# Performance work log

Measured on AMD Instinct MI355X. Metric: run time of the kernel, lower is better.

## Reference

```python
import jax, jax.numpy as jnp
import numpy as np

C = 256
RED = 8
D = C // RED  # qk dim = 32
EPS = 1e-5   # nn.LayerNorm default


def setup_inputs() -> dict:
    key = jax.random.key(0)
    ks = jax.random.split(key, 10)
    B, H, W = 4, 64, 64
    s = 0.02
    return {
        "x": jax.random.normal(ks[0], (B, C, H, W), dtype=jnp.float32),
        "wq": jax.random.normal(ks[1], (D, C), dtype=jnp.float32) * s,
        "bq": jax.random.normal(ks[2], (D,), dtype=jnp.float32) * s,
        "wk": jax.random.normal(ks[3], (D, C), dtype=jnp.float32) * s,
        "bk": jax.random.normal(ks[4], (D,), dtype=jnp.float32) * s,
        "wv": jax.random.normal(ks[5], (C, C), dtype=jnp.float32) * s,
        "bv": jax.random.normal(ks[6], (C,), dtype=jnp.float32) * s,
        "gamma": jax.random.normal(ks[7], (1,), dtype=jnp.float32) * 0.1,
        "ln_w": jnp.ones((C,), dtype=jnp.float32),
        "ln_b": jnp.zeros((C,), dtype=jnp.float32),
    }


def reference(x, wq, bq, wk, bk, wv, bv, gamma, ln_w, ln_b):
    B, Cc, H, W = x.shape
    N = H * W
    xf = x.reshape(B, Cc, N)  # [B,C,N]
    # 1x1 convs == per-pixel linear over channels
    q = jnp.einsum('dc,bcn->bnd', wq, xf) + bq              # [B,N,D]
    k = jnp.einsum('dc,bcn->bdn', wk, xf) + bk[:, None]     # [B,D,N]
    v = jnp.einsum('ec,bcn->ben', wv, xf) + bv[:, None]     # [B,C,N]
    scale = 1.0 / (D ** 0.5)
    scores = jnp.einsum('bnd,bdm->bnm', q, k) * scale       # [B,N,N]
    # original subtracts row max then softmax; jax.nn.softmax is equivalent & stable
    attn = jax.nn.softmax(scores, axis=-1)                  # [B,N,N]
    out = jnp.einsum('bcm,bnm->bcn', v, attn)               # [B,C,N]
    res = gamma[0] * out + xf                               # gamma residual
    # LayerNorm over channel dim (module permutes to channels-last)
    r = res.transpose(0, 2, 1)                              # [B,N,C]
    mu = jnp.mean(r, axis=-1, keepdims=True)
    var = jnp.mean(jnp.square(r - mu), axis=-1, keepdims=True)
    y = (r - mu) * jax.lax.rsqrt(var + EPS) * ln_w + ln_b
    return y.transpose(0, 2, 1).reshape(B, Cc, H, W)
```

## Files before the change

### kernel.cpp

```cpp
#include <hip/hip_runtime.h>
#include <hip/hip_bf16.h>

#define NPIX 4096
#define NCH  256

typedef __attribute__((ext_vector_type(8))) short short8;
typedef __attribute__((ext_vector_type(4))) short s16x4;
typedef __attribute__((ext_vector_type(16))) float f32x16;
typedef __attribute__((ext_vector_type(8))) int i32x8;

union Frag64 { long l[4]; i32x8 v; };

#define SC1 0x7F7F7F7F

__device__ inline unsigned int pkfp8x4(float a, float b, float c, float d) {
    int w = __builtin_amdgcn_cvt_pk_fp8_f32(a, b, 0, false);
    w = __builtin_amdgcn_cvt_pk_fp8_f32(c, d, w, true);
    return (unsigned int)w;
}

__device__ inline unsigned char fp8b(float a) {
    return (unsigned char)(__builtin_amdgcn_cvt_pk_fp8_f32(a, a, 0, false) & 0xff);
}

__device__ inline float bperm(int srclane, float v) {
    return __int_as_float(__builtin_amdgcn_ds_bpermute(
        srclane << 2, __float_as_int(v)));
}

__device__ inline unsigned short bfbits(float f) {
    __hip_bfloat16 h = __float2bfloat16(f);
    return *reinterpret_cast<unsigned short*>(&h);
}

#if __has_builtin(__builtin_amdgcn_exp2f)
__device__ inline float exp2_raw(float x) { return __builtin_amdgcn_exp2f(x); }
#else
__device__ inline float exp2_raw(float x) { return __builtin_exp2f(x); }
#endif

__device__ inline void barrier_nodrain() {
    __builtin_amdgcn_sched_barrier(0);
    asm volatile("s_waitcnt lgkmcnt(0)" ::: "memory");
    __builtin_amdgcn_s_barrier();
    __builtin_amdgcn_sched_barrier(0);
}

__global__ void __launch_bounds__(256) prep_kernel(
    const float* __restrict__ x,
    const float* __restrict__ wq, const float* __restrict__ bq,
    const float* __restrict__ wk, const float* __restrict__ bk,
    const float* __restrict__ wv, const float* __restrict__ bv,
    __hip_bfloat16* __restrict__ Wc, float* __restrict__ bc,
    __hip_bfloat16* __restrict__ XTg)
{
    const int bid = blockIdx.x;
    const int t   = threadIdx.x;
    if (bid >= 1024) {
        const int j = bid - 1024;
        const float kQ = 0.17677669529663687f * 1.4426950408889634f;
        const float* src;
        float sc = 1.0f;
        if (j < 32)       { src = wq + j * 256; }
        else if (j < 64)  { src = wk + (j - 32) * 256; sc = kQ; }
        else              { src = wv + (j - 64) * 256; }
        Wc[j * 256 + t] = __float2bfloat16(src[t] * sc);
        if (t == 0) {
            float bb = (j < 32) ? bq[j] : (j < 64) ? bk[j - 32] * kQ : bv[j - 64];
            bc[j] = bb;
        }
        return;
    }
    __shared__ float xs[64][65];
    const int b  = bid >> 8;
    const int c0 = ((bid >> 6) & 3) * 64;
    const int n0 = (bid & 63) * 64;
    const float* xb = x + ((size_t)b * NCH + c0) * NPIX + n0;
    #pragma unroll
    for (int i = 0; i < 4; ++i) {
        int c  = i * 16 + (t >> 4);
        int n4 = (t & 15) * 4;
        float4 v = *(const float4*)(xb + (size_t)c * NPIX + n4);
        xs[c][n4 + 0] = v.x;
        xs[c][n4 + 1] = v.y;
        xs[c][n4 + 2] = v.z;
        xs[c][n4 + 3] = v.w;
    }
    __syncthreads();
    #pragma unroll
    for (int i = 0; i < 4; ++i) {
        int nn  = i * 16 + (t >> 4);
        int cL4 = (t & 15) * 4;
        s16x4 w;
        w.x = (short)bfbits(xs[cL4 + 0][nn]);
        w.y = (short)bfbits(xs[cL4 + 1][nn]);
        w.z = (short)bfbits(xs[cL4 + 2][nn]);
        w.w = (short)bfbits(xs[cL4 + 3][nn]);
        *(s16x4*)(XTg + ((size_t)b * NPIX + n0 + nn) * NCH + c0 + cL4) = w;
    }
}

__global__ void __launch_bounds__(256) proj_kernel(
    const __hip_bfloat16* __restrict__ Wc, const float* __restrict__ bc,
    const __hip_bfloat16* __restrict__ XTg,
    unsigned char* __restrict__ Q8, unsigned char* __restrict__ K8,
    unsigned char* __restrict__ V8)
{
    const int b    = blockIdx.z;
    const int t    = threadIdx.x;
    const int lane = t & 63;
    const int wid  = t >> 6;
    const int lo   = lane & 31;
    const int hi   = lane >> 5;
    const int n0   = blockIdx.x * 128 + wid * 32;
    const int jb   = blockIdx.y * 2;

    short8 xf[16];
    const __hip_bfloat16* xr = XTg + ((size_t)b * NPIX + n0 + lo) * NCH;
    #pragma unroll
    for (int ks = 0; ks < 16; ++ks)
        xf[ks] = *(const short8*)(xr + ks * 16 + hi * 8);

    #pragma unroll
    for (int jo = 0; jo < 2; ++jo) {
        const int jt = jb + jo;
        f32x16 acc;
        #pragma unroll
        for (int r = 0; r < 16; ++r) acc[r] = 0.f;
        const __hip_bfloat16* wr = Wc + (size_t)(jt * 32 + lo) * NCH;
        #pragma unroll
        for (int ks = 0; ks < 16; ++ks) {
            short8 wf = *(const short8*)(wr + ks * 16 + hi * 8);
            acc = __builtin_amdgcn_mfma_f32_32x32x16_bf16(wf, xf[ks], acc, 0, 0, 0);
        }
        if (jt < 2) {
            unsigned char* dst = (jt == 0 ? Q8 : K8)
                               + ((size_t)b * NPIX + n0 + lo) * 32;
            #pragma unroll
            for (int g = 0; g < 4; ++g) {
                int jr = 8 * g + 4 * hi;
                unsigned int w = pkfp8x4(acc[4 * g + 0] + bc[jt * 32 + jr + 0],
                                         acc[4 * g + 1] + bc[jt * 32 + jr + 1],
                                         acc[4 * g + 2] + bc[jt * 32 + jr + 2],
                                         acc[4 * g + 3] + bc[jt * 32 + jr + 3]);
                *(unsigned int*)(dst + jr) = w;
            }
        } else {
            unsigned char* vb = V8 + (size_t)b * NPIX * NCH
                              + (size_t)((n0 + lo) >> 4) * 4096 + (lo & 15);
            #pragma unroll
            for (int r = 0; r < 16; ++r) {
                int jr = (r & 3) + 8 * (r >> 2) + 4 * hi;
                int c  = jt * 32 + jr - 64;
                vb[(size_t)c * 16] = fp8b(acc[r] + bc[jt * 32 + jr]);
            }
        }
    }
}

__global__ void __launch_bounds__(512, 4) attn_kernel(
    const unsigned char* __restrict__ Q8, const unsigned char* __restrict__ K8,
    const unsigned char* __restrict__ V8, const __hip_bfloat16* __restrict__ XTg,
    const float* __restrict__ gamma_p, const float* __restrict__ lnw,
    const float* __restrict__ lnb, float* __restrict__ out)
{
    __shared__ char smem[39936];

    const int t    = threadIdx.x;
    const int lane = t & 63;
    const int wid  = __builtin_amdgcn_readfirstlane(t >> 6);
    const int lo   = lane & 31;
    const int hi   = lane >> 5;

    const int lid = blockIdx.y * 128 + blockIdx.x;
    const int xcd = lid & 7;
    const int b   = xcd >> 1;
    const int q0  = ((xcd & 1) * 64 + (lid >> 3)) * 32;

    const unsigned char* Qb = Q8 + ((size_t)b * NPIX + q0) * 32;
    Frag64 qv;
    qv.l[0] = *(const long*)(Qb + lo * 32 + hi * 8);
    qv.l[1] = *(const long*)(Qb + lo * 32 + 16 + hi * 8);
    qv.l[2] = 0; qv.l[3] = 0;

    const unsigned char* Ku = K8 + (size_t)b * NPIX * 32 + wid * 1024;
    const int koff = lo * 32 + hi * 8;
    const unsigned char* Vu = V8 + (size_t)b * NPIX * NCH + wid * 512;
    const int vloff = lo * 16 + hi * 8;

    unsigned int rva[16];
    #pragma unroll
    for (int s = 0; s < 4; ++s)
        #pragma unroll
        for (int p = 0; p < 4; ++p)
            rva[4 * s + p] = (unsigned)(lo * 256
                           + (((8 * s + 2 * p + hi) ^ (lo & 15)) << 3));
    unsigned int wva[4];
    #pragma unroll
    for (int g = 0; g < 4; ++g)
        wva[g] = (unsigned)(lo * 256 + 4 * hi
               + (((4 * wid + g) ^ (lo & 15)) << 3));

    f32x16 acc;
    #pragma unroll
    for (int r = 0; r < 16; ++r) acc[r] = 0.f;
    float s_run = 0.f;

    Frag64 ka;
    ka.l[0] = *(const long*)(Ku + koff);
    ka.l[1] = *(const long*)(Ku + koff + 16);
    ka.l[2] = 0; ka.l[3] = 0;
    long kB0 = 0, kB1 = 0;

    Frag64 vva[4];
    #pragma unroll
    for (int s = 0; s < 4; ++s)
        #pragma unroll
        for (int p = 0; p < 4; ++p)
            vva[s].l[p] = *(const long*)(Vu + (4 * s + p) * 4096 + vloff);

    {
        f32x16 sct;
        #pragma unroll
        for (int r = 0; r < 16; ++r) sct[r] = 0.f;
        sct = __builtin_amdgcn_mfma_scale_f32_32x32x64_f8f6f4(
            ka.v, qv.v, sct, 0, 0, 0, SC1, 0, SC1);
        kB0 = *(const long*)(Ku + 8192 + koff);
        kB1 = *(const long*)(Ku + 8192 + koff + 16);
        float psum = 0.f;
        #pragma unroll
        for (int g = 0; g < 4; ++g) {
            float e0 = exp2_raw(sct[4 * g + 0]);
            float e1 = exp2_raw(sct[4 * g + 1]);
            float e2 = exp2_raw(sct[4 * g + 2]);
            float e3 = exp2_raw(sct[4 * g + 3]);
            psum += (e0 + e1) + (e2 + e3);
            *(unsigned int*)(smem + wva[g]) = pkfp8x4(e0, e1, e2, e3);
        }
        s_run += psum;
    }
    barrier_nodrain();

    for (int it = 1; it < 16; ++it) {
        #pragma unroll
        for (int g = 0; g < 4; ++g) wva[g] ^= 8192u;

        ka.l[0] = kB0; ka.l[1] = kB1;
        f32x16 sct;
        #pragma unroll
        for (int r = 0; r < 16; ++r) sct[r] = 0.f;
        sct = __builtin_amdgcn_mfma_scale_f32_32x32x64_f8f6f4(
            ka.v, qv.v, sct, 0, 0, 0, SC1, 0, SC1);

        __builtin_amdgcn_s_setprio(1);
        #pragma unroll
        for (int s = 0; s < 4; ++s) {
            Frag64 pa;
            #pragma unroll
            for (int p = 0; p < 4; ++p)
                pa.l[p] = *(const long*)(smem + rva[4 * s + p]);
            acc = __builtin_amdgcn_mfma_scale_f32_32x32x64_f8f6f4(
                pa.v, vva[s].v, acc, 0, 0, 0, SC1, 0, SC1);
        }
        __builtin_amdgcn_s_setprio(0);

        if (it < 15) {
            const unsigned char* kn = Ku + (size_t)(it + 1) * 8192;
            kB0 = *(const long*)(kn + koff);
            kB1 = *(const long*)(kn + koff + 16);
        }

        const unsigned char* vit = Vu + (size_t)it * 65536;
        #pragma unroll
        for (int s = 0; s < 4; ++s)
            #pragma unroll
            for (int p = 0; p < 4; ++p)
                vva[s].l[p] = *(const long*)(vit + (4 * s + p) * 4096 + vloff);

        float psum = 0.f;
        #pragma unroll
        for (int g = 0; g < 4; ++g) {
            float e0 = exp2_raw(sct[4 * g + 0]);
            float e1 = exp2_raw(sct[4 * g + 1]);
            float e2 = exp2_raw(sct[4 * g + 2]);
            float e3 = exp2_raw(sct[4 * g + 3]);
            psum += (e0 + e1) + (e2 + e3);
            *(unsigned int*)(smem + wva[g]) = pkfp8x4(e0, e1, e2, e3);
        }
        s_run += psum;

        barrier_nodrain();

        #pragma unroll
        for (int i = 0; i < 16; ++i) rva[i] ^= 8192u;
    }

    {
        __builtin_amdgcn_s_setprio(1);
        #pragma unroll
        for (int s = 0; s < 4; ++s) {
            Frag64 pa;
            #pragma unroll
            for (int p = 0; p < 4; ++p)
                pa.l[p] = *(const long*)(smem + rva[4 * s + p]);
            acc = __builtin_amdgcn_mfma_scale_f32_32x32x64_f8f6f4(
                pa.v, vva[s].v, acc, 0, 0, 0, SC1, 0, SC1);
        }
        __builtin_amdgcn_s_setprio(0);
    }

    s_run += __shfl_xor(s_run, 32);

    float* red_sp = (float*)(smem + 36864);
    float* red2p  = (float*)(smem + 37888);
    float (*ybuf)[36] = (float(*)[36])smem;

    if (hi == 0) red_sp[wid * 32 + lo] = s_run;
    __syncthreads();
    float stot = 0.f;
    #pragma unroll
    for (int w = 0; w < 8; ++w) stot += red_sp[w * 32 + lo];
    const float invs = 1.0f / stot;
    const float gamma = gamma_p[0];
    const int cL = 32 * wid + lo;
    const __hip_bfloat16* XTb = XTg + ((size_t)b * NPIX + q0) * NCH + cL;
    float rv[16];
    #pragma unroll
    for (int r = 0; r < 16; ++r) {
        int qr = (r & 3) + 8 * (r >> 2) + 4 * hi;
        float ir = bperm(qr, invs);
        float xv = __bfloat162float(XTb[(size_t)qr * NCH]);
        rv[r] = gamma * (acc[r] * ir) + xv;
        float s1 = rv[r];
        float s2 = rv[r] * rv[r];
        #pragma unroll
        for (int off = 1; off < 32; off <<= 1) {
            s1 += __shfl_xor(s1, off);
            s2 += __shfl_xor(s2, off);
        }
        if (lo == 0) {
            red2p[qr * 16 + wid * 2]     = s1;
            red2p[qr * 16 + wid * 2 + 1] = s2;
        }
    }
    __syncthreads();
    float sA = 0.f, sB = 0.f;
    #pragma unroll
    for (int w = 0; w < 8; ++w) {
        sA += red2p[lo * 16 + w * 2];
        sB += red2p[lo * 16 + w * 2 + 1];
    }
    const float mean = sA * (1.f / 256.f);
    const float var  = sB * (1.f / 256.f) - mean * mean;
    const float rstd = rsqrtf(var + 1e-5f);
    const float lwv = lnw[cL];
    const float lbv = lnb[cL];
    #pragma unroll
    for (int r = 0; r < 16; ++r) {
        int qr = (r & 3) + 8 * (r >> 2) + 4 * hi;
        float m  = bperm(qr, mean);
        float rr = bperm(qr, rstd);
        ybuf[cL][qr] = (rv[r] - m) * rr * lwv + lbv;
    }
    __syncthreads();
    const int c_r = t >> 1;
    const int qh  = (t & 1) * 16;
    float* dst = out + ((size_t)b * NCH + c_r) * NPIX + q0 + qh;
    #pragma unroll
    for (int j = 0; j < 4; ++j) {
        float4 v;
        v.x = ybuf[c_r][qh + j * 4 + 0];
        v.y = ybuf[c_r][qh + j * 4 + 1];
        v.z = ybuf[c_r][qh + j * 4 + 2];
        v.w = ybuf[c_r][qh + j * 4 + 3];
        *(float4*)(dst + j * 4) = v;
    }
}

extern "C" void kernel_launch(void* const* d_in, const int* in_sizes, int n_in,
                              void* d_out, int out_size, void* d_ws, size_t ws_size,
                              hipStream_t stream) {
    const float* x     = (const float*)d_in[0];
    const float* wq    = (const float*)d_in[1];
    const float* bq    = (const float*)d_in[2];
    const float* wk    = (const float*)d_in[3];
    const float* bk    = (const float*)d_in[4];
    const float* wv    = (const float*)d_in[5];
    const float* bv    = (const float*)d_in[6];
    const float* gamma = (const float*)d_in[7];
    const float* ln_w  = (const float*)d_in[8];
    const float* ln_b  = (const float*)d_in[9];
    float* out = (float*)d_out;

    const int B = 4;
    unsigned char* ws = (unsigned char*)d_ws;
    unsigned char*  Q8 = ws;
    unsigned char*  K8 = ws + (512u << 10);
    unsigned char*  V8 = ws + (1u << 20);
    __hip_bfloat16* XT = (__hip_bfloat16*)(ws + (5u << 20));
    __hip_bfloat16* Wc = (__hip_bfloat16*)(ws + (13u << 20));
    float*          bc = (float*)(ws + (13u << 20) + 163840);

    prep_kernel<<<dim3(1344), 256, 0, stream>>>(x, wq, bq, wk, bk, wv, bv,
                                                Wc, bc, XT);
    proj_kernel<<<dim3(32, 5, B), 256, 0, stream>>>(Wc, bc, XT, Q8, K8, V8);
    attn_kernel<<<dim3(128, B), 512, 0, stream>>>(Q8, K8, V8, XT, gamma,
                                                  ln_w, ln_b, out);
}
```

Measured before the change: 85.91 us.

## Process two key sub-blocks per barrier stage to halve synchronization count

The attention main loop now handles 512 keys per stage instead of 256, running two QK MFMA/exp sub-steps and two PV sub-steps between barriers, so it takes 8 iterations instead of 16. The K prefetch covers two fragments and the LDS probability buffer doubles its row stride and double-buffer offset. The aim is to halve the block barriers and the per-stage overhead, and to interleave more independent work for latency hiding. In exchange it uses more LDS and registers, which may lower occupancy and pushes the scratch reduction region close to the larger buffer.

Measured after the change: 119.4 us. 38.9% more time.

```diff
diff --git a/kernel.cpp b/kernel.cpp
--- a/kernel.cpp
+++ b/kernel.cpp
@@ -183,50 +183,56 @@
     qv.l[1] = *(const long*)(Qb + lo * 32 + 16 + hi * 8);
     qv.l[2] = 0; qv.l[3] = 0;
 
-    const unsigned char* Ku = K8 + (size_t)b * NPIX * 32 + wid * 1024;
+    const unsigned char* Ku = K8 + (size_t)b * NPIX * 32 + wid * 2048;
     const int koff = lo * 32 + hi * 8;
     const unsigned char* Vu = V8 + (size_t)b * NPIX * NCH + wid * 512;
     const int vloff = lo * 16 + hi * 8;
 
+    const int swz = lo & 15;
     unsigned int rva[16];
     #pragma unroll
     for (int s = 0; s < 4; ++s)
         #pragma unroll
         for (int p = 0; p < 4; ++p)
-            rva[4 * s + p] = (unsigned)(lo * 256
-                           + (((8 * s + 2 * p + hi) ^ (lo & 15)) << 3));
-    unsigned int wva[4];
-    #pragma unroll
-    for (int g = 0; g < 4; ++g)
-        wva[g] = (unsigned)(lo * 256 + 4 * hi
-               + (((4 * wid + g) ^ (lo & 15)) << 3));
+            rva[4 * s + p] = (unsigned)(lo * 512
+                           + (((8 * s + 2 * p + hi) ^ swz) << 3));
+    unsigned int wva[8];
+    #pragma unroll
+    for (int g = 0; g < 8; ++g)
+        wva[g] = (unsigned)(lo * 512 + 4 * hi
+               + (((8 * wid + g) ^ swz) << 3));
 
     f32x16 acc;
     #pragma unroll
     for (int r = 0; r < 16; ++r) acc[r] = 0.f;
     float s_run = 0.f;
 
-    Frag64 ka;
-    ka.l[0] = *(const long*)(Ku + koff);
-    ka.l[1] = *(const long*)(Ku + koff + 16);
-    ka.l[2] = 0; ka.l[3] = 0;
-    long kB0 = 0, kB1 = 0;
+    Frag64 ka0, ka1;
+    ka0.l[0] = *(const long*)(Ku + koff);
+    ka0.l[1] = *(const long*)(Ku + koff + 16);
+    ka0.l[2] = 0; ka0.l[3] = 0;
+    ka1.l[0] = *(const long*)(Ku + 1024 + koff);
+    ka1.l[1] = *(const long*)(Ku + 1024 + koff + 16);
+    ka1.l[2] = 0; ka1.l[3] = 0;
+    long kB0 = 0, kB1 = 0, kB2 = 0, kB3 = 0;
 
     Frag64 vva[4];
     #pragma unroll
     for (int s = 0; s < 4; ++s)
         #pragma unroll
         for (int p = 0; p < 4; ++p)
-            vva[s].l[p] = *(const long*)(Vu + (4 * s + p) * 4096 + vloff);
+            vva[s].l[p] = *(const long*)(Vu + s * 16384 + p * 4096 + vloff);
 
     {
         f32x16 sct;
         #pragma unroll
         for (int r = 0; r < 16; ++r) sct[r] = 0.f;
         sct = __builtin_amdgcn_mfma_scale_f32_32x32x64_f8f6f4(
-            ka.v, qv.v, sct, 0, 0, 0, SC1, 0, SC1);
-        kB0 = *(const long*)(Ku + 8192 + koff);
-        kB1 = *(const long*)(Ku + 8192 + koff + 16);
+            ka0.v, qv.v, sct, 0, 0, 0, SC1, 0, SC1);
+        kB0 = *(const long*)(Ku + 16384 + koff);
+        kB1 = *(const long*)(Ku + 16384 + koff + 16);
+        kB2 = *(const long*)(Ku + 16384 + 1024 + koff);
+        kB3 = *(const long*)(Ku + 16384 + 1024 + koff + 16);
         float psum = 0.f;
         #pragma unroll
         for (int g = 0; g < 4; ++g) {
@@ -237,20 +243,35 @@
             psum += (e0 + e1) + (e2 + e3);
             *(unsigned int*)(smem + wva[g]) = pkfp8x4(e0, e1, e2, e3);
         }
-        s_run += psum;
-    }
-    barrier_nodrain();
-
-    for (int it = 1; it < 16; ++it) {
-        #pragma unroll
-        for (int g = 0; g < 4; ++g) wva[g] ^= 8192u;
-
-        ka.l[0] = kB0; ka.l[1] = kB1;
-        f32x16 sct;
         #pragma unroll
         for (int r = 0; r < 16; ++r) sct[r] = 0.f;
         sct = __builtin_amdgcn_mfma_scale_f32_32x32x64_f8f6f4(
-            ka.v, qv.v, sct, 0, 0, 0, SC1, 0, SC1);
+            ka1.v, qv.v, sct, 0, 0, 0, SC1, 0, SC1);
+        #pragma unroll
+        for (int g = 0; g < 4; ++g) {
+            float e0 = exp2_raw(sct[4 * g + 0]);
+            float e1 = exp2_raw(sct[4 * g + 1]);
+            float e2 = exp2_raw(sct[4 * g + 2]);
+            float e3 = exp2_raw(sct[4 * g + 3]);
+            psum += (e0 + e1) + (e2 + e3);
+            *(unsigned int*)(smem + wva[4 + g]) = pkfp8x4(e0, e1, e2, e3);
+        }
+        s_run += psum;
+    }
+    barrier_nodrain();
+
+    for (int it = 1; it < 8; ++it) {
+        #pragma unroll
+        for (int g = 0; g < 8; ++g) wva[g] ^= 16384u;
+
+        ka0.l[0] = kB0; ka0.l[1] = kB1;
+        ka1.l[0] = kB2; ka1.l[1] = kB3;
+
+        f32x16 sct;
+        #pragma unroll
+        for (int r = 0; r < 16; ++r) sct[r] = 0.f;
+        sct = __builtin_amdgcn_mfma_scale_f32_32x32x64_f8f6f4(
+            ka0.v, qv.v, sct, 0, 0, 0, SC1, 0, SC1);
 
         __builtin_amdgcn_s_setprio(1);
         #pragma unroll
@@ -264,18 +285,14 @@
         }
         __builtin_amdgcn_s_setprio(0);
 
-        if (it < 15) {
-            const unsigned char* kn = Ku + (size_t)(it + 1) * 8192;
-            kB0 = *(const long*)(kn + koff);
-            kB1 = *(const long*)(kn + koff + 16);
-        }
-
-        const unsigned char* vit = Vu + (size_t)it * 65536;
-        #pragma unroll
-        for (int s = 0; s < 4; ++s)
-            #pragma unroll
-            for (int p = 0; p < 4; ++p)
-                vva[s].l[p] = *(const long*)(vit + (4 * s + p) * 4096 + vloff);
+        {
+            const unsigned char* vb1 = Vu + (size_t)(it - 1) * 131072 + 65536;
+            #pragma unroll
+            for (int s = 0; s < 4; ++s)
+                #pragma unroll
+                for (int p = 0; p < 4; ++p)
+                    vva[s].l[p] = *(const long*)(vb1 + s * 16384 + p * 4096 + vloff);
+        }
 
         float psum = 0.f;
         #pragma unroll
@@ -287,12 +304,56 @@
             psum += (e0 + e1) + (e2 + e3);
             *(unsigned int*)(smem + wva[g]) = pkfp8x4(e0, e1, e2, e3);
         }
+
+        #pragma unroll
+        for (int r = 0; r < 16; ++r) sct[r] = 0.f;
+        sct = __builtin_amdgcn_mfma_scale_f32_32x32x64_f8f6f4(
+            ka1.v, qv.v, sct, 0, 0, 0, SC1, 0, SC1);
+
+        __builtin_amdgcn_s_setprio(1);
+        #pragma unroll
+        for (int s = 0; s < 4; ++s) {
+            Frag64 pa;
+            #pragma unroll
+            for (int p = 0; p < 4; ++p)
+                pa.l[p] = *(const long*)(smem + rva[4 * s + p] + 256);
+            acc = __builtin_amdgcn_mfma_scale_f32_32x32x64_f8f6f4(
+                pa.v, vva[s].v, acc, 0, 0, 0, SC1, 0, SC1);
+        }
+        __builtin_amdgcn_s_setprio(0);
+
+        {
+            const unsigned char* vb0 = Vu + (size_t)it * 131072;
+            #pragma unroll
+            for (int s = 0; s < 4; ++s)
+                #pragma unroll
+                for (int p = 0; p < 4; ++p)
+                    vva[s].l[p] = *(const long*)(vb0 + s * 16384 + p * 4096 + vloff);
+        }
+
+        #pragma unroll
+        for (int g = 0; g < 4; ++g) {
+            float e0 = exp2_raw(sct[4 * g + 0]);
+            float e1 = exp2_raw(sct[4 * g + 1]);
+            float e2 = exp2_raw(sct[4 * g + 2]);
+            float e3 = exp2_raw(sct[4 * g + 3]);
+            psum += (e0 + e1) + (e2 + e3);
+            *(unsigned int*)(smem + wva[4 + g]) = pkfp8x4(e0, e1, e2, e3);
+        }
         s_run += psum;
 
+        if (it < 7) {
+            const unsigned char* kn = Ku + (size_t)(it + 1) * 16384;
+            kB0 = *(const long*)(kn + koff);
+            kB1 = *(const long*)(kn + koff + 16);
+            kB2 = *(const long*)(kn + 1024 + koff);
+            kB3 = *(const long*)(kn + 1024 + koff + 16);
+        }
+
         barrier_nodrain();
 
         #pragma unroll
-        for (int i = 0; i < 16; ++i) rva[i] ^= 8192u;
+        for (int i = 0; i < 16; ++i) rva[i] ^= 16384u;
     }
 
     {
@@ -303,6 +364,23 @@
             #pragma unroll
             for (int p = 0; p < 4; ++p)
                 pa.l[p] = *(const long*)(smem + rva[4 * s + p]);
+            acc = __builtin_amdgcn_mfma_scale_f32_32x32x64_f8f6f4(
+                pa.v, vva[s].v, acc, 0, 0, 0, SC1, 0, SC1);
+        }
+        __builtin_amdgcn_s_setprio(0);
+        const unsigned char* vb1 = Vu + (size_t)7 * 131072 + 65536;
+        #pragma unroll
+        for (int s = 0; s < 4; ++s)
+            #pragma unroll
+            for (int p = 0; p < 4; ++p)
+                vva[s].l[p] = *(const long*)(vb1 + s * 16384 + p * 4096 + vloff);
+        __builtin_amdgcn_s_setprio(1);
+        #pragma unroll
+        for (int s = 0; s < 4; ++s) {
+            Frag64 pa;
+            #pragma unroll
+            for (int p = 0; p < 4; ++p)
+                pa.l[p] = *(const long*)(smem + rva[4 * s + p] + 256);
             acc = __builtin_amdgcn_mfma_scale_f32_32x32x64_f8f6f4(
                 pa.v, vva[s].v, acc, 0, 0, 0, SC1, 0, SC1);
         }
```
